# Kernel tuning notes

Measured on AMD Instinct MI355X. Metric: run time of the kernel, lower is better.

## Reference

```python
import jax, jax.numpy as jnp
import numpy as np

L, N, D = 1024, 64, 1024  # seq_len, batch, d_model (= hidden)


def setup_inputs() -> dict:
    key = jax.random.key(0)
    k1, k2, k3 = jax.random.split(key, 3)
    x = jax.random.normal(k1, (L, N, D), dtype=jnp.float32)
    # flax OptimizedLSTMCell params: input kernel (no bias), recurrent kernel + bias,
    # gates packed as [i, f, g, o] along last dim.
    Wi = jax.random.normal(k2, (D, 4 * D), dtype=jnp.float32) / np.float32(np.sqrt(D))
    Wh = jax.random.normal(k3, (D, 4 * D), dtype=jnp.float32) / np.float32(np.sqrt(D))
    b = jnp.zeros((4 * D,), dtype=jnp.float32)
    return {"x": x, "Wi": Wi, "Wh": Wh, "b": b}


def reference(x, Wi, Wh, b):
    # x: [L, N, D]; scan LSTM cell over time axis 0 (matches nn.scan in_axes=0).
    d = Wh.shape[0]
    n = x.shape[1]
    # Input projections have no carry dependency: batch them in one big GEMM.
    xW = jnp.einsum('lnd,df->lnf', x, Wi)  # [L, N, 4D]

    def step(carry, xw_t):
        c, h = carry
        y = xw_t + h @ Wh + b  # [N, 4D]
        i, f, g, o = jnp.split(y, 4, axis=-1)
        i = jax.nn.sigmoid(i)
        f = jax.nn.sigmoid(f)
        g = jnp.tanh(g)
        o = jax.nn.sigmoid(o)
        c_new = f * c + i * g
        h_new = o * jnp.tanh(c_new)
        return (c_new, h_new), h_new

    c0 = jnp.zeros((n, d), dtype=x.dtype)
    h0 = jnp.zeros((n, d), dtype=x.dtype)
    _, hs = jax.lax.scan(step, (c0, h0), xW)
    return hs  # [L, N, D]
```

## Files before the change

kernel.cpp:

```cpp
#include <hip/hip_runtime.h>
#include <stdint.h>

#define LSEQ 1024
#define NB   64
#define DM   1024
#define FOURD 4096

typedef float f32x4 __attribute__((ext_vector_type(4)));
typedef short short8_t __attribute__((ext_vector_type(8)));
typedef __bf16 bf16x8 __attribute__((ext_vector_type(8)));

__device__ __forceinline__ unsigned short f2bf(float f) {
    unsigned int u = __builtin_bit_cast(unsigned int, f);
    u += 0x7fffu + ((u >> 16) & 1u);
    return (unsigned short)(u >> 16);
}

__device__ __forceinline__ f32x4 mfma16(short8_t a, short8_t b, f32x4 c) {
    return __builtin_amdgcn_mfma_f32_16x16x32_bf16(
        __builtin_bit_cast(bf16x8, a), __builtin_bit_cast(bf16x8, b), c, 0, 0, 0);
}

__global__ void init_ws_kernel(unsigned int* __restrict__ p, int n) {
    int i = blockIdx.x * blockDim.x + threadIdx.x;
    int stride = gridDim.x * blockDim.x;
    for (; i < n; i += stride) p[i] = 0u;
}

__global__ void convert_x_kernel(const float4* __restrict__ src, uint4* __restrict__ dst) {
    size_t i = (size_t)blockIdx.x * blockDim.x + threadIdx.x;
    float4 a = src[2 * i];
    float4 b = src[2 * i + 1];
    uint4 r;
    r.x = (unsigned)f2bf(a.x) | ((unsigned)f2bf(a.y) << 16);
    r.y = (unsigned)f2bf(a.z) | ((unsigned)f2bf(a.w) << 16);
    r.z = (unsigned)f2bf(b.x) | ((unsigned)f2bf(b.y) << 16);
    r.w = (unsigned)f2bf(b.z) | ((unsigned)f2bf(b.w) << 16);
    dst[i] = r;
}

__global__ void prep_w_kernel(const float* __restrict__ W,
                              unsigned short* __restrict__ wp) {
    const int fid = blockIdx.x * 256 + threadIdx.x;
    const int lane = fid & 63;
    const int kk = (fid >> 6) & 3;
    const int q  = (fid >> 8) & 3;
    const int ks = (fid >> 10) & 7;
    const int ug = fid >> 13;
    const int k0 = (ks << 7) + (kk << 5) + ((lane >> 4) << 3);
    const int col = (q << 10) + (ug << 4) + (lane & 15);
    short8_t v;
    #pragma unroll
    for (int j = 0; j < 8; ++j)
        v[j] = (short)f2bf(W[(size_t)(k0 + j) * FOURD + col]);
    *(short8_t*)(wp + ((size_t)fid << 3)) = v;
}

#define HL(arr, i, OFFS)                                                        \
    asm volatile("global_load_dwordx4 %0, %1, off offset:" OFFS " sc0 sc1"      \
                 : "=v"(arr[i]) : "v"(hap) : "memory")
#define XL(arr, i, OFFS)                                                        \
    asm volatile("global_load_dwordx4 %0, %1, off offset:" OFFS                 \
                 : "=v"(arr[i]) : "v"(xap) : "memory")
#define WAITV(NSTR)                                          \
    asm volatile("s_waitcnt vmcnt(" NSTR ")" ::: "memory");  \
    __builtin_amdgcn_sched_barrier(0)
#define WAITL()                                              \
    asm volatile("s_waitcnt lgkmcnt(0)" ::: "memory")
#define BARRIER()                                            \
    __builtin_amdgcn_s_barrier();                            \
    asm volatile("" ::: "memory")

__global__ __launch_bounds__(512)
__attribute__((amdgpu_waves_per_eu(2, 2)))
void lstm_scan_kernel(const unsigned short* __restrict__ wip,
                      const unsigned short* __restrict__ whp,
                      const float* __restrict__ bias,
                      const unsigned short* __restrict__ xb,
                      unsigned short* __restrict__ hbuf,
                      unsigned int* __restrict__ flags,
                      float* __restrict__ out)
{
    __shared__ float plds[8][4][16][20];
    const int tid = threadIdx.x;
    const int wg = blockIdx.x;
    const int rg = (wg & 7) >> 1;
    const int ug = (wg >> 3) | ((wg & 1) << 5);
    const int r0 = rg << 4, U0 = ug << 4;
    const int lane = tid & 63, ks = tid >> 6;
    const int la = lane & 15, kseg = lane >> 4;

    short8_t BI[4][4], BH[4][4];
    {
        const unsigned short* wb = wip + (((size_t)(ug << 3) + ks) << 13);
        const unsigned short* hb = whp + (((size_t)(ug << 3) + ks) << 13);
        #pragma unroll
        for (int q = 0; q < 4; ++q)
            #pragma unroll
            for (int kk = 0; kk < 4; ++kk) {
                BI[q][kk] = *(const short8_t*)(wb + ((((q << 2) + kk) << 6) + lane) * 8);
                BH[q][kk] = *(const short8_t*)(hb + ((((q << 2) + kk) << 6) + lane) * 8);
            }
    }

    const int aoff = (r0 + la) * DM + (ks << 7) + (kseg << 3);

    const int er = tid >> 4, eu = tid & 15;
    const float bI = bias[U0 + eu], bF = bias[1024 + U0 + eu],
                bG = bias[2048 + U0 + eu], bO = bias[3072 + U0 + eu];
    float cst = 0.0f;
    unsigned int* myflag = flags + (rg << 6) + ug;
    const unsigned int* gfp = flags + (rg << 6) + (ks << 3) + (lane & 7);

    short8_t xf[4];
    {
        const unsigned short* xap = xb + aoff;
        XL(xf, 0, "0"); XL(xf, 1, "64"); XL(xf, 2, "128"); XL(xf, 3, "192");
        asm volatile("s_waitcnt vmcnt(0)" ::: "memory");
        __builtin_amdgcn_sched_barrier(0);
    }

    for (int t = 0; t < LSEQ; ++t) {
        if (t) {
            while (true) {
                unsigned int f = __hip_atomic_load(gfp, __ATOMIC_RELAXED,
                                                   __HIP_MEMORY_SCOPE_AGENT);
                if (__all((int)(f >= (unsigned)t))) break;
                __builtin_amdgcn_s_sleep(1);
            }
        }

        short8_t hf[4];
        {
            const unsigned short* hap =
                hbuf + (size_t)((t & 1) ^ 1) * (NB * DM) + aoff;
            HL(hf, 0, "0"); HL(hf, 1, "64"); HL(hf, 2, "128"); HL(hf, 3, "192");
        }
        WAITV("4");

        f32x4 acc[4];
        #pragma unroll
        for (int q = 0; q < 4; ++q) acc[q] = (f32x4){0.f, 0.f, 0.f, 0.f};
        #pragma unroll
        for (int kk = 0; kk < 4; ++kk)
            #pragma unroll
            for (int q = 0; q < 4; ++q)
                acc[q] = mfma16(xf[kk], BI[q][kk], acc[q]);

        WAITV("0");

        #pragma unroll
        for (int kk = 0; kk < 4; ++kk)
            #pragma unroll
            for (int q = 0; q < 4; ++q)
                acc[q] = mfma16(hf[kk], BH[q][kk], acc[q]);

        #pragma unroll
        for (int q = 0; q < 4; ++q)
            *(f32x4*)&plds[ks][q][la][kseg << 2] = acc[q];
        WAITL();
        BARRIER();

        float hv = 0.f, hn = 0.f;
        if (tid < 256) {
            float vi = bI, vf = bF, vg = bG, vo = bO;
            #pragma unroll
            for (int s = 0; s < 8; ++s) {
                vi += plds[s][0][eu][er];
                vf += plds[s][1][eu][er];
                vg += plds[s][2][eu][er];
                vo += plds[s][3][eu][er];
            }
            float gi = 1.0f / (1.0f + __expf(-vi));
            float gF = 1.0f / (1.0f + __expf(-vf));
            float gg = 1.0f - 2.0f / (__expf(2.0f * vg) + 1.0f);
            float go = 1.0f / (1.0f + __expf(-vo));
            cst = gF * cst + gi * gg;
            hv = go * (1.0f - 2.0f / (__expf(2.0f * cst) + 1.0f));
            hn = __shfl_xor(hv, 1);

            if (!(eu & 1)) {
                unsigned int hp = (unsigned)f2bf(hv) | ((unsigned)f2bf(hn) << 16);
                unsigned int* hw = (unsigned int*)(hbuf + (size_t)(t & 1) * (NB * DM)
                                                   + (size_t)(r0 + er) * DM + U0 + eu);
                asm volatile("global_store_dword %0, %1, off sc0 sc1"
                             :: "v"(hw), "v"(hp) : "memory");
            }
        }

        {
            const int tn = (t < LSEQ - 1) ? t + 1 : t;
            const unsigned short* xap = xb + (size_t)tn * (NB * DM) + aoff;
            XL(xf, 0, "0"); XL(xf, 1, "64"); XL(xf, 2, "128"); XL(xf, 3, "192");
        }
        WAITV("4");

        BARRIER();

        if (tid == 0)
            __hip_atomic_store(myflag, (unsigned)(t + 1), __ATOMIC_RELAXED,
                               __HIP_MEMORY_SCOPE_AGENT);

        if (tid < 256 && !(eu & 1))
            *(float2*)(out + ((size_t)(t * NB) + r0 + er) * DM + U0 + eu)
                = make_float2(hv, hn);
    }
}

#define HM(arr, i, kk) {                                        \
    short8_t b = *(const short8_t*)(bph + (kk) * 1024);         \
    if ((kk) & 1) acc1 = mfma16(arr[i], b, acc1);               \
    else          acc0 = mfma16(arr[i], b, acc0); }

__global__ __launch_bounds__(256)
void lstm_fallback_kernel(const float* __restrict__ x,
                          const float* __restrict__ Wi,
                          const float* __restrict__ Wh,
                          const float* __restrict__ bias,
                          unsigned short* __restrict__ hbuf,
                          unsigned int* __restrict__ flags,
                          float* __restrict__ out)
{
    __shared__ short Wlds[65536];
    __shared__ float ylds[32 * 33];
    __shared__ float blds[32];

    const int tid  = threadIdx.x;
    const int wgid = blockIdx.x;
    const int g    = wgid >> 7;
    const int ug   = wgid & 127;
    const int U0   = ug << 3;
    const int rowbase = g << 5;

    {
        const int c    = tid & 31;
        const int ct_  = c >> 4;
        const int lb   = c & 15;
        const int gcol = ((c >> 3) << 10) + U0 + (c & 7);
        for (int k = tid >> 5; k < 1024; k += 8) {
            const int lane_ = lb | (((k >> 3) & 3) << 4);
            const int sidx  = (ct_ * 32 + (k >> 5)) * 512 + lane_ * 8 + (k & 7);
            Wlds[sidx]         = (short)f2bf(Wi[(size_t)k * FOURD + gcol]);
            Wlds[sidx + 32768] = (short)f2bf(Wh[(size_t)k * FOURD + gcol]);
        }
        if (tid < 32) blds[tid] = bias[((tid >> 3) << 10) + U0 + (tid & 7)];
    }
    __syncthreads();

    const int lane = tid & 63;
    const int wv   = tid >> 6;
    const int rt   = wv >> 1;
    const int ct   = wv & 1;
    const int arow = rowbase + (rt << 4) + (lane & 15);
    const int kseg = (lane >> 4) << 3;
    const char* bpx = (const char*)Wlds + ct * 32768 + lane * 16;
    const char* bph = (const char*)Wlds + 65536 + ct * 32768 + lane * 16;

    const int er = tid >> 3;
    const int eu = tid & 7;
    const float bI = blds[eu], bF = blds[8 + eu], bG = blds[16 + eu], bO = blds[24 + eu];
    float cstate = 0.0f;
    unsigned int* gflags = flags + (g << 7);

    for (int t = 0; t < LSEQ; ++t) {
        f32x4 acc0 = {0.f, 0.f, 0.f, 0.f};
        f32x4 acc1 = {0.f, 0.f, 0.f, 0.f};

        {
            const float* ap = x + ((size_t)t * NB + arow) * DM + kseg;
            #pragma unroll 4
            for (int kk = 0; kk < 32; ++kk) {
                float4 lo = *(const float4*)(ap + kk * 32);
                float4 hi = *(const float4*)(ap + kk * 32 + 4);
                short8_t a;
                a[0] = (short)f2bf(lo.x); a[1] = (short)f2bf(lo.y);
                a[2] = (short)f2bf(lo.z); a[3] = (short)f2bf(lo.w);
                a[4] = (short)f2bf(hi.x); a[5] = (short)f2bf(hi.y);
                a[6] = (short)f2bf(hi.z); a[7] = (short)f2bf(hi.w);
                short8_t b = *(const short8_t*)(bpx + kk * 1024);
                if (kk & 1) acc1 = mfma16(a, b, acc1);
                else        acc0 = mfma16(a, b, acc0);
            }
        }

        if (t && wv == 0) {
            const unsigned int* fp = gflags + (lane << 1);
            while (true) {
                unsigned int f0 = __hip_atomic_load(fp,     __ATOMIC_RELAXED, __HIP_MEMORY_SCOPE_AGENT);
                unsigned int f1 = __hip_atomic_load(fp + 1, __ATOMIC_RELAXED, __HIP_MEMORY_SCOPE_AGENT);
                int ok = (f0 >= (unsigned)t) && (f1 >= (unsigned)t);
                if (__all(ok)) break;
                __builtin_amdgcn_s_sleep(1);
            }
        }
        __syncthreads();

        {
            const unsigned short* hap =
                hbuf + (size_t)((t & 1) ^ 1) * (NB * DM) + (size_t)arow * DM + kseg;
            short8_t A0[8], A1[8];
            HL(A0,0,"0");    HL(A0,1,"64");   HL(A0,2,"128");  HL(A0,3,"192");
            HL(A0,4,"256");  HL(A0,5,"320");  HL(A0,6,"384");  HL(A0,7,"448");
            HL(A1,0,"512");  HL(A1,1,"576");  HL(A1,2,"640");  HL(A1,3,"704");
            HL(A1,4,"768");  HL(A1,5,"832");  HL(A1,6,"896");  HL(A1,7,"960");
            WAITV("8");
            HM(A0,0,0)  HM(A0,1,1)  HM(A0,2,2)  HM(A0,3,3)
            HM(A0,4,4)  HM(A0,5,5)  HM(A0,6,6)  HM(A0,7,7)
            HL(A0,0,"1024"); HL(A0,1,"1088"); HL(A0,2,"1152"); HL(A0,3,"1216");
            HL(A0,4,"1280"); HL(A0,5,"1344"); HL(A0,6,"1408"); HL(A0,7,"1472");
            WAITV("8");
            HM(A1,0,8)  HM(A1,1,9)  HM(A1,2,10) HM(A1,3,11)
            HM(A1,4,12) HM(A1,5,13) HM(A1,6,14) HM(A1,7,15)
            HL(A1,0,"1536"); HL(A1,1,"1600"); HL(A1,2,"1664"); HL(A1,3,"1728");
            HL(A1,4,"1792"); HL(A1,5,"1856"); HL(A1,6,"1920"); HL(A1,7,"1984");
            WAITV("8");
            HM(A0,0,16) HM(A0,1,17) HM(A0,2,18) HM(A0,3,19)
            HM(A0,4,20) HM(A0,5,21) HM(A0,6,22) HM(A0,7,23)
            WAITV("0");
            HM(A1,0,24) HM(A1,1,25) HM(A1,2,26) HM(A1,3,27)
            HM(A1,4,28) HM(A1,5,29) HM(A1,6,30) HM(A1,7,31)
        }

        {
            f32x4 acc = acc0 + acc1;
            const int rr0 = (rt << 4) + ((lane >> 4) << 2);
            const int c0 = (ct << 4) + (lane & 15);
            #pragma unroll
            for (int j = 0; j < 4; ++j) ylds[(rr0 + j) * 33 + c0] = acc[j];
        }
        __syncthreads();

        {
            const float* yr = ylds + er * 33;
            float vi = yr[eu]      + bI;
            float vf = yr[8 + eu]  + bF;
            float vg = yr[16 + eu] + bG;
            float vo = yr[24 + eu] + bO;
            float gi = 1.0f / (1.0f + __expf(-vi));
            float gF = 1.0f / (1.0f + __expf(-vf));
            float gg = 1.0f - 2.0f / (__expf(2.0f * vg) + 1.0f);
            float go = 1.0f / (1.0f + __expf(-vo));
            cstate = gF * cstate + gi * gg;
            float hv = go * (1.0f - 2.0f / (__expf(2.0f * cstate) + 1.0f));
            float hvn = __shfl_down(hv, 1);
            if ((tid & 1) == 0) {
                const int n = rowbase + er;
                const int d = U0 + eu;
                unsigned int hp = (unsigned)f2bf(hv) | ((unsigned)f2bf(hvn) << 16);
                unsigned int* hw = (unsigned int*)(hbuf + (size_t)(t & 1) * (NB * DM)
                                                   + (size_t)n * DM + d);
                __hip_atomic_store(hw, hp, __ATOMIC_RELAXED, __HIP_MEMORY_SCOPE_AGENT);
                *(float2*)(out + ((size_t)t * NB + n) * DM + d) = make_float2(hv, hvn);
            }
        }
        asm volatile("s_waitcnt vmcnt(0)" ::: "memory");
        __syncthreads();

        if (tid == 0) {
            __hip_atomic_store(gflags + ug, (unsigned)(t + 1),
                               __ATOMIC_RELAXED, __HIP_MEMORY_SCOPE_AGENT);
            asm volatile("s_waitcnt vmcnt(0)" ::: "memory");
        }
    }
}

extern "C" void kernel_launch(void* const* d_in, const int* in_sizes, int n_in,
                              void* d_out, int out_size, void* d_ws, size_t ws_size,
                              hipStream_t stream) {
    (void)in_sizes; (void)n_in; (void)out_size;
    const float* x  = (const float*)d_in[0];
    const float* Wi = (const float*)d_in[1];
    const float* Wh = (const float*)d_in[2];
    const float* b  = (const float*)d_in[3];
    float* out = (float*)d_out;

    char* ws = (char*)d_ws;
    const size_t OFF_HB  = 4096;
    const size_t OFF_WIP = OFF_HB + 262144;
    const size_t OFF_WHP = OFF_WIP + 8388608ull;
    const size_t OFF_XB  = OFF_WHP + 8388608ull;
    const size_t NEED    = OFF_XB + 134217728ull;

    unsigned int*   flags = (unsigned int*)ws;
    unsigned short* hbuf  = (unsigned short*)(ws + OFF_HB);

    init_ws_kernel<<<64, 256, 0, stream>>>((unsigned int*)ws, 66560);

    if (ws_size >= NEED) {
        unsigned short* wip = (unsigned short*)(ws + OFF_WIP);
        unsigned short* whp = (unsigned short*)(ws + OFF_WHP);
        unsigned short* xb  = (unsigned short*)(ws + OFF_XB);
        convert_x_kernel<<<32768, 256, 0, stream>>>((const float4*)x, (uint4*)xb);
        prep_w_kernel<<<2048, 256, 0, stream>>>(Wi, wip);
        prep_w_kernel<<<2048, 256, 0, stream>>>(Wh, whp);
        lstm_scan_kernel<<<256, 512, 0, stream>>>(wip, whp, b, xb, hbuf, flags, out);
    } else {
        lstm_fallback_kernel<<<256, 256, 0, stream>>>(x, Wi, Wh, b, hbuf, flags, out);
    }
}
```

Baseline: 3.783 ms.

## Replace per-block barrier+flag with per-wave flags and double-buffered LDS partials

Each of the four writer waves now publishes its own step flag right after its h stores drain. This removes the second workgroup barrier per timestep, and double-buffering the LDS partial sums keeps the next step's writes from racing the current reads. Consumers poll eight contiguous flags with two vector loads per lane instead of one scalar flag each. The flag array layout grows fourfold, which assumes the workspace is sized and zeroed accordingly. Dropping the barrier relies on per-wave vmcnt ordering for correctness.

After: 8.429 ms. +122.8%, slower.

```diff
diff --git a/kernel.cpp b/kernel.cpp
--- a/kernel.cpp
+++ b/kernel.cpp
@@ -9,6 +9,7 @@
 typedef float f32x4 __attribute__((ext_vector_type(4)));
 typedef short short8_t __attribute__((ext_vector_type(8)));
 typedef __bf16 bf16x8 __attribute__((ext_vector_type(8)));
+typedef unsigned int uint4v __attribute__((ext_vector_type(4)));
 
 __device__ __forceinline__ unsigned short f2bf(float f) {
     unsigned int u = __builtin_bit_cast(unsigned int, f);
@@ -81,7 +82,7 @@
                       unsigned int* __restrict__ flags,
                       float* __restrict__ out)
 {
-    __shared__ float plds[8][4][16][20];
+    __shared__ float plds[2][8][4][16][20];
     const int tid = threadIdx.x;
     const int wg = blockIdx.x;
     const int rg = (wg & 7) >> 1;
@@ -109,8 +110,8 @@
     const float bI = bias[U0 + eu], bF = bias[1024 + U0 + eu],
                 bG = bias[2048 + U0 + eu], bO = bias[3072 + U0 + eu];
     float cst = 0.0f;
-    unsigned int* myflag = flags + (rg << 6) + ug;
-    const unsigned int* gfp = flags + (rg << 6) + (ks << 3) + (lane & 7);
+    unsigned int* myflag = flags + (rg << 8) + (ks << 6) + ug;
+    const unsigned int* pfp = flags + (rg << 8) + ((la >> 2) << 6) + (ks << 3);
 
     short8_t xf[4];
     {
@@ -123,11 +124,20 @@
     for (int t = 0; t < LSEQ; ++t) {
         if (t) {
             while (true) {
-                unsigned int f = __hip_atomic_load(gfp, __ATOMIC_RELAXED,
-                                                   __HIP_MEMORY_SCOPE_AGENT);
-                if (__all((int)(f >= (unsigned)t))) break;
+                uint4v f0, f1;
+                asm volatile("global_load_dwordx4 %0, %2, off sc0 sc1\n\t"
+                             "global_load_dwordx4 %1, %2, off offset:16 sc0 sc1\n\t"
+                             "s_waitcnt vmcnt(0)"
+                             : "=v"(f0), "=v"(f1) : "v"(pfp) : "memory");
+                int ok = (f0[0] >= (unsigned)t) && (f0[1] >= (unsigned)t) &&
+                         (f0[2] >= (unsigned)t) && (f0[3] >= (unsigned)t) &&
+                         (f1[0] >= (unsigned)t) && (f1[1] >= (unsigned)t) &&
+                         (f1[2] >= (unsigned)t) && (f1[3] >= (unsigned)t);
+                if (__all(ok)) break;
                 __builtin_amdgcn_s_sleep(1);
             }
+        } else {
+            WAITV("0");
         }
 
         short8_t hf[4];
@@ -136,7 +146,6 @@
                 hbuf + (size_t)((t & 1) ^ 1) * (NB * DM) + aoff;
             HL(hf, 0, "0"); HL(hf, 1, "64"); HL(hf, 2, "128"); HL(hf, 3, "192");
         }
-        WAITV("4");
 
         f32x4 acc[4];
         #pragma unroll
@@ -157,7 +166,7 @@
 
         #pragma unroll
         for (int q = 0; q < 4; ++q)
-            *(f32x4*)&plds[ks][q][la][kseg << 2] = acc[q];
+            *(f32x4*)&plds[t & 1][ks][q][la][kseg << 2] = acc[q];
         WAITL();
         BARRIER();
 
@@ -166,10 +175,10 @@
             float vi = bI, vf = bF, vg = bG, vo = bO;
             #pragma unroll
             for (int s = 0; s < 8; ++s) {
-                vi += plds[s][0][eu][er];
-                vf += plds[s][1][eu][er];
-                vg += plds[s][2][eu][er];
-                vo += plds[s][3][eu][er];
+                vi += plds[t & 1][s][0][eu][er];
+                vf += plds[t & 1][s][1][eu][er];
+                vg += plds[t & 1][s][2][eu][er];
+                vo += plds[t & 1][s][3][eu][er];
             }
             float gi = 1.0f / (1.0f + __expf(-vi));
             float gF = 1.0f / (1.0f + __expf(-vf));
@@ -193,17 +202,18 @@
             const unsigned short* xap = xb + (size_t)tn * (NB * DM) + aoff;
             XL(xf, 0, "0"); XL(xf, 1, "64"); XL(xf, 2, "128"); XL(xf, 3, "192");
         }
-        WAITV("4");
-
-        BARRIER();
-
-        if (tid == 0)
-            __hip_atomic_store(myflag, (unsigned)(t + 1), __ATOMIC_RELAXED,
-                               __HIP_MEMORY_SCOPE_AGENT);
-
-        if (tid < 256 && !(eu & 1))
-            *(float2*)(out + ((size_t)(t * NB) + r0 + er) * DM + U0 + eu)
-                = make_float2(hv, hn);
+
+        if (tid < 256) {
+            WAITV("4");
+            if ((tid & 63) == 0) {
+                unsigned int tv = (unsigned)(t + 1);
+                asm volatile("global_store_dword %0, %1, off sc0 sc1"
+                             :: "v"(myflag), "v"(tv) : "memory");
+            }
+            if (!(eu & 1))
+                *(float2*)(out + ((size_t)(t * NB) + r0 + er) * DM + U0 + eu)
+                    = make_float2(hv, hn);
+        }
     }
 }
 
```
